# Optimization experiments

Measured on AMD Instinct MI355X. Metric: run time of the kernel, lower is better.

## Reference

```python
import jax, jax.numpy as jnp
import numpy as np

N = 262144      # nodes
E = 1048576     # edges
NC = 30         # node feature dim
ED = 13         # bond (edge) feature dim
H = 256         # hidden_channels
GH = 512        # config.gnn_hidden_channels
OUT = 256       # out_channels
L = 4           # num_layers
G = 8192        # num graphs in batch


def setup_inputs() -> dict:
    key = jax.random.key(0)
    ks = jax.random.split(key, 16)
    inp = {
        "x": jax.random.normal(ks[0], (N, NC), jnp.float32),
        "edge_attr": jax.random.normal(ks[1], (E, ED), jnp.float32),
        "edge_index": jax.random.randint(ks[2], (2, E), 0, N, jnp.int64),
        "batch": jnp.sort(jax.random.randint(ks[3], (N,), 0, G, jnp.int64)),
        # node_to_hid: Linear(NC, H)
        "W_nh": jax.random.normal(ks[4], (NC, H), jnp.float32) / np.sqrt(NC),
        "b_nh": jnp.zeros((H,), jnp.float32),
        # shared GINEConv nn: Linear(H, H) + ReLU (same module instance for every layer)
        "W1": jax.random.normal(ks[5], (H, H), jnp.float32) / np.sqrt(H),
        "b1": jnp.zeros((H,), jnp.float32),
        # per-layer edge projection Linear(ED, H) inside each GINEConv
        "We": jax.random.normal(ks[6], (L, ED, H), jnp.float32) / np.sqrt(ED),
        "be": jnp.zeros((L, H), jnp.float32),
        # lin1: H -> GH, lin2: GH -> OUT
        "Wl1": jax.random.normal(ks[7], (H, GH), jnp.float32) / np.sqrt(H),
        "bl1": jnp.zeros((GH,), jnp.float32),
        "Wl2": jax.random.normal(ks[8], (GH, OUT), jnp.float32) / np.sqrt(GH),
        "bl2": jnp.zeros((OUT,), jnp.float32),
    }
    return inp


def reference(x, edge_attr, W_nh, b_nh, W1, b1, We, be, Wl1, bl1, Wl2, bl2,
              edge_index, batch):
    src = edge_index[0]  # x_j (messages flow source -> target)
    dst = edge_index[1]
    hid = x @ W_nh + b_nh                                   # [N, H]
    for l in range(L):
        e = edge_attr @ We[l] + be[l]                       # [E, H]
        msg = jax.nn.relu(hid[src] + e)                     # gather + fuse
        agg = jax.ops.segment_sum(msg, dst, num_segments=N) # scatter-sum
        # GINEConv (eps=0) -> shared nn (Linear+ReLU), then outer relu in forward
        hid = jax.nn.relu(jax.nn.relu((hid + agg) @ W1 + b1))
    out = jax.nn.relu(hid @ Wl1 + bl1) @ Wl2 + bl2          # [N, OUT]
    # global_add_pool readout
    return jax.ops.segment_sum(out, batch, num_segments=G)  # [G, OUT]
```

## Files before the change

### kernel.cpp

```cpp
#include <hip/hip_runtime.h>
#include <hip/hip_bf16.h>

#define N_NODES 262144
#define N_EDGES 1048576
#define NC      30
#define ED      13
#define H       256
#define GH      512
#define OUT_C   256
#define NLAYERS 4
#define NGRAPHS 8192

typedef __hip_bfloat16 bf16;
typedef __attribute__((ext_vector_type(8))) short short8;
typedef __attribute__((ext_vector_type(4))) float f32x4;

__device__ unsigned short g_W1t[H * H];
__device__ unsigned short g_Wl1t[2][H * H];
__device__ unsigned short g_Wl2t[2][H * H];
__device__ float g_b1[H];
__device__ float g_bl1[GH];
__device__ float g_bl2[OUT_C];
__device__ unsigned int g_ssrc[N_EDGES];
__device__ float        g_seat[N_EDGES * 16];
__device__ unsigned int g_rowptr[N_NODES + 1];
__device__ unsigned int g_cursor[N_NODES];
__device__ unsigned int g_bsum[1024];

__device__ __forceinline__ float hw2f(unsigned short h) {
    return __uint_as_float(((unsigned int)h) << 16);
}
__device__ __forceinline__ float ldf(const void* p, size_t i, bool isbf) {
    return isbf ? hw2f(((const unsigned short*)p)[i]) : ((const float*)p)[i];
}
__device__ __forceinline__ int ldi(const void* p, size_t j, bool is64) {
    return ((const int*)p)[is64 ? 2 * j : j];
}
__device__ __forceinline__ unsigned short bfbits(float f) {
    bf16 b = __float2bfloat16(f);
    return *(unsigned short*)&b;
}
__device__ __forceinline__ float lo16(unsigned int u) { return __uint_as_float(u << 16); }
__device__ __forceinline__ float hi16(unsigned int u) { return __uint_as_float(u & 0xFFFF0000u); }
__device__ __forceinline__ unsigned int pk2(float a, float b) {
    return (unsigned int)bfbits(a) | ((unsigned int)bfbits(b) << 16);
}
__device__ __forceinline__ bool sniff_bf16(const void* xv) {
    const unsigned short* q = (const unsigned short*)xv;
    int c = 0;
    for (int i = 0; i < 32; ++i) {
        unsigned short h = q[2 * i];
        int e = (h >> 7) & 0xFF;
        c += (h == 0 || (e >= 97 && e <= 141)) ? 1 : 0;
    }
    return c >= 20;
}
__device__ __forceinline__ bool sniff_i64(const void* pv, size_t baseWord) {
    const unsigned int* q = (const unsigned int*)pv;
    int z = 0;
    for (int i = 0; i < 32; ++i) z += (q[baseWord + 2 * i + 1] == 0) ? 1 : 0;
    return z >= 20;
}
__device__ __forceinline__ void gload_lds16(const void* g, void* l) {
    __builtin_amdgcn_global_load_lds(
        (const __attribute__((address_space(1))) unsigned int*)g,
        (__attribute__((address_space(3))) unsigned int*)l, 16, 0, 0);
}

__global__ __launch_bounds__(256) void fill_f4(float4* p, int n4, float val) {
    int i = blockIdx.x * 256 + threadIdx.x;
    int stride = gridDim.x * 256;
    float4 z = make_float4(val, val, val, val);
    for (; i < n4; i += stride) p[i] = z;
}

__global__ __launch_bounds__(256) void pack_wt(const void* __restrict__ in,
        int ldin, int k0, int n0, int which) {
    const bool isbf = sniff_bf16(in);
    unsigned short* outp = which == 0 ? g_W1t
                         : which == 1 ? g_Wl1t[0]
                         : which == 2 ? g_Wl1t[1]
                         : which == 3 ? g_Wl2t[0] : g_Wl2t[1];
    const int n = blockIdx.x, k = threadIdx.x;
    outp[(n << 8) + k] = bfbits(ldf(in, (size_t)(k0 + k) * ldin + n0 + n, isbf));
}
__global__ __launch_bounds__(256) void pack_bias(const void* b1, const void* bl1,
                                                 const void* bl2) {
    const int t = threadIdx.x;
    const bool s1 = sniff_bf16(b1), s2 = sniff_bf16(bl1), s3 = sniff_bf16(bl2);
    g_b1[t]        = ldf(b1,  t,       s1);
    g_bl1[t]       = ldf(bl1, t,       s2);
    g_bl1[t + 256] = ldf(bl1, t + 256, s2);
    g_bl2[t]       = ldf(bl2, t,       s3);
}

__global__ __launch_bounds__(256) void csr_zero() {
    g_cursor[blockIdx.x * 256 + threadIdx.x] = 0u;
}
__global__ __launch_bounds__(256) void hist_dst(const void* __restrict__ eidx) {
    const bool is64 = sniff_i64(eidx, 0);
    const int e = blockIdx.x * 256 + threadIdx.x;
    int dst = ldi(eidx, (size_t)N_EDGES + e, is64);
    if ((unsigned)dst >= (unsigned)N_NODES) dst = 0;
    atomicAdd(&g_cursor[dst], 1u);
}
__global__ __launch_bounds__(256) void scan1() {
    __shared__ unsigned int sh[256];
    const int tid = threadIdx.x;
    sh[tid] = g_cursor[blockIdx.x * 256 + tid];
    __syncthreads();
    for (int s = 128; s > 0; s >>= 1) {
        if (tid < s) sh[tid] += sh[tid + s];
        __syncthreads();
    }
    if (tid == 0) g_bsum[blockIdx.x] = sh[0];
}
__global__ __launch_bounds__(256) void scan2() {
    __shared__ unsigned int sh[1024];
    const int tid = threadIdx.x;
    for (int j = tid; j < 1024; j += 256) sh[j] = g_bsum[j];
    __syncthreads();
    if (tid == 0) {
        unsigned int run = 0;
        for (int j = 0; j < 1024; ++j) { unsigned int t = sh[j]; sh[j] = run; run += t; }
    }
    __syncthreads();
    for (int j = tid; j < 1024; j += 256) g_bsum[j] = sh[j];
}
__global__ __launch_bounds__(256) void scan3() {
    __shared__ unsigned int sh[256];
    const int tid = threadIdx.x;
    const int i = blockIdx.x * 256 + tid;
    const unsigned int v = g_cursor[i];
    sh[tid] = v;
    __syncthreads();
    for (int ofs = 1; ofs < 256; ofs <<= 1) {
        unsigned int t = (tid >= ofs) ? sh[tid - ofs] : 0u;
        __syncthreads();
        sh[tid] += t;
        __syncthreads();
    }
    const unsigned int excl = sh[tid] - v + g_bsum[blockIdx.x];
    g_rowptr[i] = excl;
    g_cursor[i] = excl;
    if (i == N_NODES - 1) g_rowptr[N_NODES] = excl + v;
}
__global__ __launch_bounds__(256) void scatter_e(
        const void* __restrict__ eidx, const void* __restrict__ eattr) {
    const bool is64 = sniff_i64(eidx, 0);
    const bool isbf = sniff_bf16(eattr);
    const int e = blockIdx.x * 256 + threadIdx.x;
    int src = ldi(eidx, e, is64);
    int dst = ldi(eidx, (size_t)N_EDGES + e, is64);
    if ((unsigned)src >= (unsigned)N_NODES) src = 0;
    if ((unsigned)dst >= (unsigned)N_NODES) dst = 0;
    unsigned int pos = atomicAdd(&g_cursor[dst], 1u);
    if (pos >= (unsigned)N_EDGES) return;
    g_ssrc[pos] = (unsigned int)src;
    float a[16];
#pragma unroll
    for (int k = 0; k < ED; ++k) a[k] = ldf(eattr, (size_t)e * ED + k, isbf);
    a[13] = 0.f; a[14] = 0.f; a[15] = 0.f;
    float* so = g_seat + (size_t)pos * 16;
#pragma unroll
    for (int k = 0; k < 4; ++k)
        *(float4*)(so + 4 * k) = *(float4*)(a + 4 * k);
}

__global__ __launch_bounds__(256) void node_proj(
        const void* __restrict__ x, const void* __restrict__ W,
        const void* __restrict__ b, bf16* __restrict__ hid) {
    const bool isbf = sniff_bf16(x);
    __shared__ float xs[16 * NC];
    const int m0 = blockIdx.x * 16;
    for (int i = threadIdx.x; i < 16 * NC; i += 256)
        xs[i] = ldf(x, (size_t)m0 * NC + i, isbf);
    __syncthreads();
    const int col = threadIdx.x;
    float w[NC];
#pragma unroll
    for (int k = 0; k < NC; ++k) w[k] = ldf(W, (size_t)k * H + col, isbf);
    const float bias = ldf(b, col, isbf);
#pragma unroll 4
    for (int r = 0; r < 16; ++r) {
        float acc = bias;
#pragma unroll
        for (int k = 0; k < NC; ++k) acc += xs[r * NC + k] * w[k];
        hid[(size_t)(m0 + r) * H + col] = __float2bfloat16(acc);
    }
}

__global__ __launch_bounds__(256, 4) void gine_agg(
        const void* __restrict__ We, size_t weOff,
        const void* __restrict__ be, size_t beOff,
        const unsigned short* __restrict__ hid,
        unsigned short* __restrict__ hsum) {
    const bool isbf = sniff_bf16(We);
    const int lane = threadIdx.x & 63;
    const int wave = threadIdx.x >> 6;
    const int wh   = wave & 1;
    const int wp   = wave >> 1;
    const int c0 = 128 * wh + 2 * lane;
    float w0[ED], w1[ED];
#pragma unroll
    for (int k = 0; k < ED; ++k) {
        const size_t o = weOff + (size_t)k * H;
        w0[k] = ldf(We, o + c0,     isbf);
        w1[k] = ldf(We, o + c0 + 1, isbf);
    }
    const float bb0 = ldf(be, beOff + c0,     isbf);
    const float bb1 = ldf(be, beOff + c0 + 1, isbf);

    const int nbase = blockIdx.x * 16 + wp * 8;
    for (int j = 0; j < 8; ++j) {
        const int node = nbase + j;
        const unsigned int r0 = __builtin_amdgcn_readfirstlane(g_rowptr[node]);
        const unsigned int r1 = __builtin_amdgcn_readfirstlane(g_rowptr[node + 1]);
        const unsigned int hu = *(const unsigned int*)(hid + (size_t)node * H + c0);
        float a0 = lo16(hu);
        float a1 = hi16(hu);
        unsigned int e = r0;
        for (; e + 2 <= r1; e += 2) {
            const unsigned int sA = __builtin_amdgcn_readfirstlane(g_ssrc[e]);
            const unsigned int sB = __builtin_amdgcn_readfirstlane(g_ssrc[e + 1]);
            const float* pA = g_seat + (size_t)e * 16;
            const float* pB = pA + 16;
            const unsigned int hA = *(const unsigned int*)(hid + (size_t)sA * H + c0);
            const unsigned int hB = *(const unsigned int*)(hid + (size_t)sB * H + c0);
            const float4 fA0 = *(const float4*)(pA);
            const float4 fA1 = *(const float4*)(pA + 4);
            const float4 fA2 = *(const float4*)(pA + 8);
            const float  fAc = pA[12];
            const float4 fB0 = *(const float4*)(pB);
            const float4 fB1 = *(const float4*)(pB + 4);
            const float4 fB2 = *(const float4*)(pB + 8);
            const float  fBc = pB[12];
            const float afA[ED] = {fA0.x, fA0.y, fA0.z, fA0.w, fA1.x, fA1.y,
                                   fA1.z, fA1.w, fA2.x, fA2.y, fA2.z, fA2.w, fAc};
            const float afB[ED] = {fB0.x, fB0.y, fB0.z, fB0.w, fB1.x, fB1.y,
                                   fB1.z, fB1.w, fB2.x, fB2.y, fB2.z, fB2.w, fBc};
            float mA0 = bb0, mA1 = bb1, mB0 = bb0, mB1 = bb1;
#pragma unroll
            for (int k = 0; k < ED; ++k) {
                mA0 += afA[k] * w0[k];
                mA1 += afA[k] * w1[k];
                mB0 += afB[k] * w0[k];
                mB1 += afB[k] * w1[k];
            }
            a0 += fmaxf(mA0 + lo16(hA), 0.f) + fmaxf(mB0 + lo16(hB), 0.f);
            a1 += fmaxf(mA1 + hi16(hA), 0.f) + fmaxf(mB1 + hi16(hB), 0.f);
        }
        if (e < r1) {
            const unsigned int s = __builtin_amdgcn_readfirstlane(g_ssrc[e]);
            const float* sp = g_seat + (size_t)e * 16;
            const unsigned int hs = *(const unsigned int*)(hid + (size_t)s * H + c0);
            const float4 f0 = *(const float4*)(sp);
            const float4 f1 = *(const float4*)(sp + 4);
            const float4 f2 = *(const float4*)(sp + 8);
            const float  fc = sp[12];
            const float af[ED] = {f0.x, f0.y, f0.z, f0.w, f1.x, f1.y, f1.z,
                                  f1.w, f2.x, f2.y, f2.z, f2.w, fc};
            float m0 = bb0, m1 = bb1;
#pragma unroll
            for (int k = 0; k < ED; ++k) {
                m0 += af[k] * w0[k];
                m1 += af[k] * w1[k];
            }
            a0 += fmaxf(m0 + lo16(hs), 0.f);
            a1 += fmaxf(m1 + hi16(hs), 0.f);
        }
        *(unsigned int*)(hsum + (size_t)node * H + c0) = pk2(a0, a1);
    }
}

template <int MODE>
__global__ __launch_bounds__(256, 4) void gemm_mfma(
        const unsigned short* __restrict__ A, int bsel,
        unsigned short* __restrict__ Cb, float* __restrict__ Cf,
        const void* __restrict__ batch, size_t batOff, int doRelu, int useBias) {
    __shared__ unsigned short As[64 * 64];
    __shared__ unsigned short Bs[256 * 64];
    const int tid  = threadIdx.x;
    const int lane = tid & 63;
    const int wave = tid >> 6;
    const int m0   = blockIdx.x * 64;

    const unsigned short* Bt = bsel == 0 ? g_W1t
                             : bsel == 1 ? g_Wl1t[0]
                             : bsel == 2 ? g_Wl1t[1]
                             : bsel == 3 ? g_Wl2t[0] : g_Wl2t[1];
    const float* bias = bsel == 0 ? g_b1
                      : bsel == 1 ? g_bl1
                      : bsel == 2 ? g_bl1 + 256 : g_bl2;

    const int ar   = tid >> 2;
    const int ac   = (tid & 3) << 4;
    const int awb  = (ar << 7) + (ac << 1);
    const int aswz = (ar & 7) << 4;
    const size_t arow = (size_t)(m0 + ar) * H + ac;
    const int nrow = lane >> 3;
    const int kbu  = ((lane & 7) ^ nrow) << 4;

    f32x4 acc0[8], acc1[8];
    const f32x4 zz = {0.f, 0.f, 0.f, 0.f};
#pragma unroll
    for (int i = 0; i < 8; ++i) { acc0[i] = zz; acc1[i] = zz; }

    const int fr   = lane & 15;
    const int fg   = lane >> 4;
    const int rowb = (wave >> 1) << 5;
    const int colb = (wave & 1) << 7;

    for (int kt = 0; kt < 4; ++kt) {
#pragma unroll
        for (int j = 0; j < 8; ++j) {
            const int q = (wave << 3) + j;
            gload_lds16((const char*)Bt + (((size_t)(q << 3) + nrow) << 9)
                            + (kt << 7) + kbu,
                        (char*)Bs + (q << 10));
        }
        {
            const size_t aoff = arow + (kt << 6);
            uint4 w0 = *(const uint4*)(A + aoff);
            uint4 w1 = *(const uint4*)(A + aoff + 8);
            *(uint4*)((char*)As + (awb ^ aswz)) = w0;
            *(uint4*)((char*)As + ((awb + 16) ^ aswz)) = w1;
        }
        __syncthreads();
#pragma unroll
        for (int s = 0; s < 2; ++s) {
            const int kofs = (s << 6) + (fg << 4);
            const int r0 = rowb + fr;
            short8 aF0 = *(const short8*)((const char*)As +
                          ((r0 << 7) + (kofs ^ ((r0 & 7) << 4))));
            short8 aF1 = *(const short8*)((const char*)As +
                          (((r0 + 16) << 7) + (kofs ^ ((r0 & 7) << 4))));
#pragma unroll
            for (int ct = 0; ct < 8; ++ct) {
                const int cc = colb + (ct << 4) + fr;
                short8 bF = *(const short8*)((const char*)Bs +
                             ((cc << 7) + (kofs ^ ((cc & 7) << 4))));
                acc0[ct] = __builtin_amdgcn_mfma_f32_16x16x32_bf16(aF0, bF, acc0[ct], 0, 0, 0);
                acc1[ct] = __builtin_amdgcn_mfma_f32_16x16x32_bf16(aF1, bF, acc1[ct], 0, 0, 0);
            }
        }
        __syncthreads();
    }

    const int crow = m0 + rowb + (fg << 2);
    if (MODE == 0) {
#pragma unroll
        for (int ct = 0; ct < 8; ++ct) {
            const int cc = colb + (ct << 4) + fr;
            const float bc = bias[cc];
#pragma unroll
            for (int r = 0; r < 4; ++r) {
                float v0 = acc0[ct][r] + bc;
                float v1 = acc1[ct][r] + bc;
                if (doRelu) { v0 = fmaxf(v0, 0.f); v1 = fmaxf(v1, 0.f); }
                Cb[(size_t)(crow + r) * H + cc]      = bfbits(v0);
                Cb[(size_t)(crow + 16 + r) * H + cc] = bfbits(v1);
            }
        }
    } else {
        const bool is64 = sniff_i64(batch, N_NODES / 2);
        int ga[5], gb[5];
#pragma unroll
        for (int r = 0; r < 4; ++r) {
            int g0 = ldi(batch, batOff + crow + r, is64);
            int g1 = ldi(batch, batOff + crow + 16 + r, is64);
            ga[r] = ((unsigned)g0 < (unsigned)NGRAPHS) ? g0 : 0;
            gb[r] = ((unsigned)g1 < (unsigned)NGRAPHS) ? g1 : 0;
        }
#pragma unroll
        for (int ct = 0; ct < 8; ++ct) {
            const int cc = colb + (ct << 4) + fr;
            const float bc = useBias ? bias[cc] : 0.f;
            float run0 = 0.f, run1 = 0.f;
#pragma unroll
            for (int r = 0; r < 4; ++r) {
                run0 += acc0[ct][r] + bc;
                if (r == 3 || ga[r + 1] != ga[r]) {
                    atomicAdd(&Cf[(size_t)ga[r] * OUT_C + cc], run0); run0 = 0.f;
                }
                run1 += acc1[ct][r] + bc;
                if (r == 3 || gb[r + 1] != gb[r]) {
                    atomicAdd(&Cf[(size_t)gb[r] * OUT_C + cc], run1); run1 = 0.f;
                }
            }
        }
    }
}

extern "C" void kernel_launch(void* const* d_in, const int* in_sizes, int n_in,
                              void* d_out, int out_size, void* d_ws, size_t ws_size,
                              hipStream_t stream) {
    const void *x = nullptr, *eattr = nullptr, *eidx = nullptr, *batch = nullptr;
    const void *W_nh = nullptr, *W1 = nullptr, *We = nullptr, *be = nullptr;
    const void *Wl1 = nullptr, *Wl2 = nullptr, *bl1 = nullptr;
    const void *z256[3] = {nullptr, nullptr, nullptr};
    int nz = 0;
    for (int i = 0; i < n_in; ++i) {
        switch (in_sizes[i]) {
            case N_NODES * NC:     x     = d_in[i]; break;
            case N_EDGES * ED:     eattr = d_in[i]; break;
            case 2 * N_EDGES:      eidx  = d_in[i]; break;
            case N_NODES:          batch = d_in[i]; break;
            case NC * H:           W_nh  = d_in[i]; break;
            case H * H:            W1    = d_in[i]; break;
            case NLAYERS * ED * H: We    = d_in[i]; break;
            case NLAYERS * H:      be    = d_in[i]; break;
            case H * GH:           if (!Wl1) Wl1 = d_in[i]; else Wl2 = d_in[i]; break;
            case GH:               bl1   = d_in[i]; break;
            case H:                if (nz < 3) z256[nz++] = d_in[i]; break;
            default: break;
        }
    }
    const void* b_nh = z256[0];
    const void* b1   = (nz > 1) ? z256[1] : z256[0];
    const void* bl2  = (nz > 2) ? z256[2] : z256[0];
    float* out = (float*)d_out;

    if (!x || !eattr || !eidx || !batch || !W_nh || !W1 || !We || !be ||
        !Wl1 || !Wl2 || !bl1 || !b_nh) {
        fill_f4<<<1024, 256, 0, stream>>>((float4*)out, NGRAPHS * OUT_C / 4, 2.0e6f);
        return;
    }

    const size_t NH = (size_t)N_NODES * H;
    const size_t need = NH * 2 + NH * 2;
    if (ws_size < need) {
        fill_f4<<<1024, 256, 0, stream>>>((float4*)out, NGRAPHS * OUT_C / 4, 1.0e6f);
        return;
    }
    bf16* hid            = (bf16*)d_ws;
    unsigned short* hsum = (unsigned short*)((char*)d_ws + NH * 2);

    pack_wt<<<256, 256, 0, stream>>>(W1,  H,     0,   0, 0);
    pack_wt<<<256, 256, 0, stream>>>(Wl1, GH,    0,   0, 1);
    pack_wt<<<256, 256, 0, stream>>>(Wl1, GH,    0, 256, 2);
    pack_wt<<<256, 256, 0, stream>>>(Wl2, OUT_C, 0,   0, 3);
    pack_wt<<<256, 256, 0, stream>>>(Wl2, OUT_C, 256, 0, 4);
    pack_bias<<<1, 256, 0, stream>>>(b1, bl1, bl2);

    csr_zero<<<N_NODES / 256, 256, 0, stream>>>();
    hist_dst<<<N_EDGES / 256, 256, 0, stream>>>(eidx);
    scan1<<<N_NODES / 256, 256, 0, stream>>>();
    scan2<<<1, 256, 0, stream>>>();
    scan3<<<N_NODES / 256, 256, 0, stream>>>();
    scatter_e<<<N_EDGES / 256, 256, 0, stream>>>(eidx, eattr);

    node_proj<<<N_NODES / 16, 256, 0, stream>>>(x, W_nh, b_nh, hid);

    for (int l = 0; l < NLAYERS; ++l) {
        gine_agg<<<N_NODES / 16, 256, 0, stream>>>(
            We, (size_t)l * ED * H, be, (size_t)l * H,
            (const unsigned short*)hid, hsum);
        gemm_mfma<0><<<N_NODES / 64, 256, 0, stream>>>(
            hsum, 0, (unsigned short*)hid, nullptr, nullptr, 0, 1, 1);
    }

    unsigned short* t0 = hsum;
    fill_f4<<<2048, 256, 0, stream>>>((float4*)out, NGRAPHS * OUT_C / 4, 0.f);
    for (int c = 0; c < 2; ++c) {
        gemm_mfma<0><<<N_NODES / 64, 256, 0, stream>>>(
            (const unsigned short*)hid, 1 + c,
            t0, nullptr, nullptr, 0, 1, 1);
        gemm_mfma<1><<<N_NODES / 64, 256, 0, stream>>>(
            t0, 3 + c,
            nullptr, out, batch, 0, 0, c == 0);
    }
}
```

Before: 2.279 ms.

## Fuse readout MLP (lin1+ReLU+lin2+pool) into one kernel keeping intermediate in LDS

```diff
diff --git a/kernel.cpp b/kernel.cpp
--- a/kernel.cpp
+++ b/kernel.cpp
@@ -208,8 +208,12 @@
         w0[k] = ldf(We, o + c0,     isbf);
         w1[k] = ldf(We, o + c0 + 1, isbf);
     }
-    const float bb0 = ldf(be, beOff + c0,     isbf);
-    const float bb1 = ldf(be, beOff + c0 + 1, isbf);
+    float bb0 = ldf(be, beOff + c0,     isbf);
+    float bb1 = ldf(be, beOff + c0 + 1, isbf);
+#pragma unroll
+    for (int k = 0; k < ED; ++k)
+        asm volatile("" : "+v"(w0[k]), "+v"(w1[k]));
+    asm volatile("" : "+v"(bb0), "+v"(bb1));
 
     const int nbase = blockIdx.x * 16 + wp * 8;
     for (int j = 0; j < 8; ++j) {
@@ -392,6 +396,139 @@
     }
 }
 
+__global__ __launch_bounds__(256, 2) void readout_fused(
+        const unsigned short* __restrict__ hid,
+        float* __restrict__ out, const void* __restrict__ batch) {
+    __shared__ unsigned short As[32 * 256];
+    __shared__ unsigned short Ts[32 * 256];
+    __shared__ unsigned short Bs[256 * 64];
+    const int tid  = threadIdx.x;
+    const int lane = tid & 63;
+    const int wave = tid >> 6;
+    const int m0   = blockIdx.x * 32;
+    const int fr   = lane & 15;
+    const int fg   = lane >> 4;
+    const int rowb = (wave >> 1) << 4;
+    const int colb = (wave & 1) << 7;
+    const int nrow = lane >> 3;
+    const int kbu  = ((lane & 7) ^ nrow) << 4;
+
+    {
+        const int rsub = lane >> 5;
+        const int koff = lane & 31;
+#pragma unroll
+        for (int qq = 0; qq < 4; ++qq) {
+            const int q = (wave << 2) + qq;
+            const int row = (q << 1) + rsub;
+            gload_lds16(hid + (size_t)(m0 + row) * H + ((koff ^ (row & 7)) << 3),
+                        (char*)Ts + 0 + (q << 10) + ((char*)As - (char*)Ts));
+        }
+    }
+
+    f32x4 oacc[8];
+    const f32x4 zz = {0.f, 0.f, 0.f, 0.f};
+#pragma unroll
+    for (int i = 0; i < 8; ++i) oacc[i] = zz;
+
+    for (int c = 0; c < 2; ++c) {
+        f32x4 tacc[8];
+#pragma unroll
+        for (int i = 0; i < 8; ++i) tacc[i] = zz;
+        const unsigned short* B1 = g_Wl1t[c];
+        for (int kt = 0; kt < 4; ++kt) {
+#pragma unroll
+            for (int j = 0; j < 8; ++j) {
+                const int q = (wave << 3) + j;
+                gload_lds16((const char*)B1 + (((size_t)(q << 3) + nrow) << 9)
+                                + (kt << 7) + kbu,
+                            (char*)Bs + (q << 10));
+            }
+            __syncthreads();
+#pragma unroll
+            for (int s = 0; s < 2; ++s) {
+                const int r0 = rowb + fr;
+                const int ka = (kt << 7) + (s << 6) + (fg << 4);
+                const short8 aF = *(const short8*)((const char*)As +
+                              (r0 << 9) + (ka ^ ((r0 & 7) << 4)));
+                const int kb = (s << 6) + (fg << 4);
+#pragma unroll
+                for (int ct = 0; ct < 8; ++ct) {
+                    const int cc = colb + (ct << 4) + fr;
+                    const short8 bF = *(const short8*)((const char*)Bs +
+                                  (cc << 7) + (kb ^ ((cc & 7) << 4)));
+                    tacc[ct] = __builtin_amdgcn_mfma_f32_16x16x32_bf16(
+                        aF, bF, tacc[ct], 0, 0, 0);
+                }
+            }
+            __syncthreads();
+        }
+#pragma unroll
+        for (int ct = 0; ct < 8; ++ct) {
+            const int cc = colb + (ct << 4) + fr;
+            const float bc = g_bl1[(c << 8) + cc];
+#pragma unroll
+            for (int r = 0; r < 4; ++r) {
+                const int row = rowb + (fg << 2) + r;
+                const float v = fmaxf(tacc[ct][r] + bc, 0.f);
+                *(unsigned short*)((char*)Ts + (row << 9) +
+                    ((cc << 1) ^ ((row & 7) << 4))) = bfbits(v);
+            }
+        }
+        __syncthreads();
+        const unsigned short* B2 = g_Wl2t[c];
+        for (int kt = 0; kt < 4; ++kt) {
+#pragma unroll
+            for (int j = 0; j < 8; ++j) {
+                const int q = (wave << 3) + j;
+                gload_lds16((const char*)B2 + (((size_t)(q << 3) + nrow) << 9)
+                                + (kt << 7) + kbu,
+                            (char*)Bs + (q << 10));
+            }
+            __syncthreads();
+#pragma unroll
+            for (int s = 0; s < 2; ++s) {
+                const int r0 = rowb + fr;
+                const int ka = (kt << 7) + (s << 6) + (fg << 4);
+                const short8 aF = *(const short8*)((const char*)Ts +
+                              (r0 << 9) + (ka ^ ((r0 & 7) << 4)));
+                const int kb = (s << 6) + (fg << 4);
+#pragma unroll
+                for (int ct = 0; ct < 8; ++ct) {
+                    const int cc = colb + (ct << 4) + fr;
+                    const short8 bF = *(const short8*)((const char*)Bs +
+                                  (cc << 7) + (kb ^ ((cc & 7) << 4)));
+                    oacc[ct] = __builtin_amdgcn_mfma_f32_16x16x32_bf16(
+                        aF, bF, oacc[ct], 0, 0, 0);
+                }
+            }
+            __syncthreads();
+        }
+    }
+
+    const bool is64 = sniff_i64(batch, N_NODES / 2);
+    const int crow = m0 + rowb + (fg << 2);
+    int ga[5];
+#pragma unroll
+    for (int r = 0; r < 4; ++r) {
+        int g0 = ldi(batch, (size_t)(crow + r), is64);
+        ga[r] = ((unsigned)g0 < (unsigned)NGRAPHS) ? g0 : 0;
+    }
+#pragma unroll
+    for (int ct = 0; ct < 8; ++ct) {
+        const int cc = colb + (ct << 4) + fr;
+        const float bc = g_bl2[cc];
+        float run = 0.f;
+#pragma unroll
+        for (int r = 0; r < 4; ++r) {
+            run += oacc[ct][r] + bc;
+            if (r == 3 || ga[r + 1] != ga[r]) {
+                atomicAdd(&out[(size_t)ga[r] * OUT_C + cc], run);
+                run = 0.f;
+            }
+        }
+    }
+}
+
 extern "C" void kernel_launch(void* const* d_in, const int* in_sizes, int n_in,
                               void* d_out, int out_size, void* d_ws, size_t ws_size,
                               hipStream_t stream) {
@@ -460,14 +597,7 @@
             hsum, 0, (unsigned short*)hid, nullptr, nullptr, 0, 1, 1);
     }
 
-    unsigned short* t0 = hsum;
     fill_f4<<<2048, 256, 0, stream>>>((float4*)out, NGRAPHS * OUT_C / 4, 0.f);
-    for (int c = 0; c < 2; ++c) {
-        gemm_mfma<0><<<N_NODES / 64, 256, 0, stream>>>(
-            (const unsigned short*)hid, 1 + c,
-            t0, nullptr, nullptr, 0, 1, 1);
-        gemm_mfma<1><<<N_NODES / 64, 256, 0, stream>>>(
-            t0, 3 + c,
-            nullptr, out, batch, 0, 0, c == 0);
-    }
-}
+    readout_fused<<<N_NODES / 32, 256, 0, stream>>>(
+        (const unsigned short*)hid, out, batch);
+}
```

Measured after the change: 2.673 ms. +17.3%, slower.

## Double-buffer GEMM LDS tiles and load A via direct global-to-LDS

Applied to the files above, without the earlier changes.

```diff
diff --git a/kernel.cpp b/kernel.cpp
--- a/kernel.cpp
+++ b/kernel.cpp
@@ -274,12 +274,12 @@
 }
 
 template <int MODE>
-__global__ __launch_bounds__(256, 4) void gemm_mfma(
+__global__ __launch_bounds__(256, 2) void gemm_mfma(
         const unsigned short* __restrict__ A, int bsel,
         unsigned short* __restrict__ Cb, float* __restrict__ Cf,
         const void* __restrict__ batch, size_t batOff, int doRelu, int useBias) {
-    __shared__ unsigned short As[64 * 64];
-    __shared__ unsigned short Bs[256 * 64];
+    __shared__ unsigned short As[2][64 * 64];
+    __shared__ unsigned short Bs[2][256 * 64];
     const int tid  = threadIdx.x;
     const int lane = tid & 63;
     const int wave = tid >> 6;
@@ -293,11 +293,6 @@
                       : bsel == 1 ? g_bl1
                       : bsel == 2 ? g_bl1 + 256 : g_bl2;
 
-    const int ar   = tid >> 2;
-    const int ac   = (tid & 3) << 4;
-    const int awb  = (ar << 7) + (ac << 1);
-    const int aswz = (ar & 7) << 4;
-    const size_t arow = (size_t)(m0 + ar) * H + ac;
     const int nrow = lane >> 3;
     const int kbu  = ((lane & 7) ^ nrow) << 4;
 
@@ -311,34 +306,43 @@
     const int rowb = (wave >> 1) << 5;
     const int colb = (wave & 1) << 7;
 
-    for (int kt = 0; kt < 4; ++kt) {
+    auto STAGE = [&](int hb, int kt) {
 #pragma unroll
         for (int j = 0; j < 8; ++j) {
             const int q = (wave << 3) + j;
             gload_lds16((const char*)Bt + (((size_t)(q << 3) + nrow) << 9)
                             + (kt << 7) + kbu,
-                        (char*)Bs + (q << 10));
-        }
-        {
-            const size_t aoff = arow + (kt << 6);
-            uint4 w0 = *(const uint4*)(A + aoff);
-            uint4 w1 = *(const uint4*)(A + aoff + 8);
-            *(uint4*)((char*)As + (awb ^ aswz)) = w0;
-            *(uint4*)((char*)As + ((awb + 16) ^ aswz)) = w1;
-        }
-        __syncthreads();
+                        (char*)Bs[hb] + (q << 10));
+        }
+#pragma unroll
+        for (int j = 0; j < 2; ++j) {
+            const int q = (wave << 1) + j;
+            gload_lds16((const char*)A + (((size_t)m0 + (q << 3) + nrow) << 9)
+                            + (kt << 7) + kbu,
+                        (char*)As[hb] + (q << 10));
+        }
+    };
+
+    STAGE(0, 0);
+    __syncthreads();
+
+    for (int kt = 0; kt < 4; ++kt) {
+        const int cur = kt & 1;
+        if (kt < 3) STAGE(cur ^ 1, kt + 1);
+        const char* asb = (const char*)As[cur];
+        const char* bsb = (const char*)Bs[cur];
 #pragma unroll
         for (int s = 0; s < 2; ++s) {
             const int kofs = (s << 6) + (fg << 4);
             const int r0 = rowb + fr;
-            short8 aF0 = *(const short8*)((const char*)As +
+            short8 aF0 = *(const short8*)(asb +
                           ((r0 << 7) + (kofs ^ ((r0 & 7) << 4))));
-            short8 aF1 = *(const short8*)((const char*)As +
+            short8 aF1 = *(const short8*)(asb +
                           (((r0 + 16) << 7) + (kofs ^ ((r0 & 7) << 4))));
 #pragma unroll
             for (int ct = 0; ct < 8; ++ct) {
                 const int cc = colb + (ct << 4) + fr;
-                short8 bF = *(const short8*)((const char*)Bs +
+                short8 bF = *(const short8*)(bsb +
                              ((cc << 7) + (kofs ^ ((cc & 7) << 4))));
                 acc0[ct] = __builtin_amdgcn_mfma_f32_16x16x32_bf16(aF0, bF, acc0[ct], 0, 0, 0);
                 acc1[ct] = __builtin_amdgcn_mfma_f32_16x16x32_bf16(aF1, bF, acc1[ct], 0, 0, 0);
```

After: 2.305 ms. About the same (+1.2%).

## Pool before final linear layer to replace per-node lin2 GEMM with per-graph GEMM

Applied to the files above, without the earlier changes.

```diff
diff --git a/kernel.cpp b/kernel.cpp
--- a/kernel.cpp
+++ b/kernel.cpp
@@ -26,6 +26,8 @@
 __device__ unsigned int g_rowptr[N_NODES + 1];
 __device__ unsigned int g_cursor[N_NODES];
 __device__ unsigned int g_bsum[1024];
+__device__ float g_P[NGRAPHS * GH];
+__device__ float g_cntf[NGRAPHS];
 
 __device__ __forceinline__ float hw2f(unsigned short h) {
     return __uint_as_float(((unsigned int)h) << 16);
@@ -72,6 +74,19 @@
     int stride = gridDim.x * 256;
     float4 z = make_float4(val, val, val, val);
     for (; i < n4; i += stride) p[i] = z;
+}
+__global__ __launch_bounds__(256) void pzero() {
+    ((float4*)g_P)[blockIdx.x * 256 + threadIdx.x] = make_float4(0.f, 0.f, 0.f, 0.f);
+}
+__global__ __launch_bounds__(256) void czero() {
+    g_cntf[blockIdx.x * 256 + threadIdx.x] = 0.f;
+}
+__global__ __launch_bounds__(256) void hist_b(const void* __restrict__ batch) {
+    const bool is64 = sniff_i64(batch, N_NODES / 2);
+    const int n = blockIdx.x * 256 + threadIdx.x;
+    int g = ldi(batch, (size_t)n, is64);
+    if ((unsigned)g >= (unsigned)NGRAPHS) g = 0;
+    atomicAdd(&g_cntf[g], 1.0f);
 }
 
 __global__ __launch_bounds__(256) void pack_wt(const void* __restrict__ in,
@@ -276,8 +291,8 @@
 template <int MODE>
 __global__ __launch_bounds__(256, 4) void gemm_mfma(
         const unsigned short* __restrict__ A, int bsel,
-        unsigned short* __restrict__ Cb, float* __restrict__ Cf,
-        const void* __restrict__ batch, size_t batOff, int doRelu, int useBias) {
+        unsigned short* __restrict__ Cb,
+        const void* __restrict__ batch, size_t batOff, int doRelu) {
     __shared__ unsigned short As[64 * 64];
     __shared__ unsigned short Bs[256 * 64];
     const int tid  = threadIdx.x;
@@ -286,12 +301,9 @@
     const int m0   = blockIdx.x * 64;
 
     const unsigned short* Bt = bsel == 0 ? g_W1t
-                             : bsel == 1 ? g_Wl1t[0]
-                             : bsel == 2 ? g_Wl1t[1]
-                             : bsel == 3 ? g_Wl2t[0] : g_Wl2t[1];
+                             : bsel == 1 ? g_Wl1t[0] : g_Wl1t[1];
     const float* bias = bsel == 0 ? g_b1
-                      : bsel == 1 ? g_bl1
-                      : bsel == 2 ? g_bl1 + 256 : g_bl2;
+                      : bsel == 1 ? g_bl1 : g_bl1 + 256;
 
     const int ar   = tid >> 2;
     const int ac   = (tid & 3) << 4;
@@ -367,29 +379,59 @@
         int ga[5], gb[5];
 #pragma unroll
         for (int r = 0; r < 4; ++r) {
-            int g0 = ldi(batch, batOff + crow + r, is64);
-            int g1 = ldi(batch, batOff + crow + 16 + r, is64);
+            int g0 = ldi(batch, (size_t)(crow + r), is64);
+            int g1 = ldi(batch, (size_t)(crow + 16 + r), is64);
             ga[r] = ((unsigned)g0 < (unsigned)NGRAPHS) ? g0 : 0;
             gb[r] = ((unsigned)g1 < (unsigned)NGRAPHS) ? g1 : 0;
         }
 #pragma unroll
         for (int ct = 0; ct < 8; ++ct) {
             const int cc = colb + (ct << 4) + fr;
-            const float bc = useBias ? bias[cc] : 0.f;
+            const float bc = bias[cc];
             float run0 = 0.f, run1 = 0.f;
 #pragma unroll
             for (int r = 0; r < 4; ++r) {
-                run0 += acc0[ct][r] + bc;
+                run0 += fmaxf(acc0[ct][r] + bc, 0.f);
                 if (r == 3 || ga[r + 1] != ga[r]) {
-                    atomicAdd(&Cf[(size_t)ga[r] * OUT_C + cc], run0); run0 = 0.f;
+                    atomicAdd(&g_P[(size_t)ga[r] * GH + batOff + cc], run0);
+                    run0 = 0.f;
                 }
-                run1 += acc1[ct][r] + bc;
+                run1 += fmaxf(acc1[ct][r] + bc, 0.f);
                 if (r == 3 || gb[r + 1] != gb[r]) {
-                    atomicAdd(&Cf[(size_t)gb[r] * OUT_C + cc], run1); run1 = 0.f;
+                    atomicAdd(&g_P[(size_t)gb[r] * GH + batOff + cc], run1);
+                    run1 = 0.f;
                 }
             }
         }
     }
+}
+
+__global__ __launch_bounds__(256) void final_out(
+        const void* __restrict__ Wl2, float* __restrict__ out) {
+    const bool isbf = sniff_bf16(Wl2);
+    __shared__ float Pl[4 * GH];
+    const int g0 = blockIdx.x * 4;
+    for (int i = threadIdx.x; i < 4 * GH; i += 256)
+        Pl[i] = g_P[(size_t)g0 * GH + i];
+    __syncthreads();
+    const int c = threadIdx.x;
+    const float b2 = g_bl2[c];
+    float a0 = g_cntf[g0]     * b2;
+    float a1 = g_cntf[g0 + 1] * b2;
+    float a2 = g_cntf[g0 + 2] * b2;
+    float a3 = g_cntf[g0 + 3] * b2;
+#pragma unroll 8
+    for (int k = 0; k < GH; ++k) {
+        const float w = ldf(Wl2, (size_t)k * OUT_C + c, isbf);
+        a0 += Pl[k] * w;
+        a1 += Pl[GH + k] * w;
+        a2 += Pl[2 * GH + k] * w;
+        a3 += Pl[3 * GH + k] * w;
+    }
+    out[(size_t)g0 * OUT_C + c]           = a0;
+    out[(size_t)(g0 + 1) * OUT_C + c]     = a1;
+    out[(size_t)(g0 + 2) * OUT_C + c]     = a2;
+    out[(size_t)(g0 + 3) * OUT_C + c]     = a3;
 }
 
 extern "C" void kernel_launch(void* const* d_in, const int* in_sizes, int n_in,
@@ -439,8 +481,6 @@
     pack_wt<<<256, 256, 0, stream>>>(W1,  H,     0,   0, 0);
     pack_wt<<<256, 256, 0, stream>>>(Wl1, GH,    0,   0, 1);
     pack_wt<<<256, 256, 0, stream>>>(Wl1, GH,    0, 256, 2);
-    pack_wt<<<256, 256, 0, stream>>>(Wl2, OUT_C, 0,   0, 3);
-    pack_wt<<<256, 256, 0, stream>>>(Wl2, OUT_C, 256, 0, 4);
     pack_bias<<<1, 256, 0, stream>>>(b1, bl1, bl2);
 
     csr_zero<<<N_NODES / 256, 256, 0, stream>>>();
@@ -457,17 +497,16 @@
             We, (size_t)l * ED * H, be, (size_t)l * H,
             (const unsigned short*)hid, hsum);
         gemm_mfma<0><<<N_NODES / 64, 256, 0, stream>>>(
-            hsum, 0, (unsigned short*)hid, nullptr, nullptr, 0, 1, 1);
-    }
-
-    unsigned short* t0 = hsum;
-    fill_f4<<<2048, 256, 0, stream>>>((float4*)out, NGRAPHS * OUT_C / 4, 0.f);
+            hsum, 0, (unsigned short*)hid, nullptr, 0, 1);
+    }
+
+    pzero<<<NGRAPHS * GH / 1024, 256, 0, stream>>>();
+    czero<<<NGRAPHS / 256, 256, 0, stream>>>();
+    hist_b<<<N_NODES / 256, 256, 0, stream>>>(batch);
     for (int c = 0; c < 2; ++c) {
-        gemm_mfma<0><<<N_NODES / 64, 256, 0, stream>>>(
+        gemm_mfma<2><<<N_NODES / 64, 256, 0, stream>>>(
             (const unsigned short*)hid, 1 + c,
-            t0, nullptr, nullptr, 0, 1, 1);
-        gemm_mfma<1><<<N_NODES / 64, 256, 0, stream>>>(
-            t0, 3 + c,
-            nullptr, out, batch, 0, 0, c == 0);
-    }
-}
+            nullptr, batch, (size_t)c * 256, 1);
+    }
+    final_out<<<NGRAPHS / 4, 256, 0, stream>>>(Wl2, out);
+}
```

Result: no change. 2.273 ms (-0.2%).
